# Optimization experiments

Measured on AMD Instinct MI355X. Metric: run time of the kernel, lower is better.

The kernel has to match this reference:

```python
import jax, jax.numpy as jnp
import numpy as np


def soft_thresholding(x, a):
    # sh(x, a) = max(0, |x| - a) * sign(x) == relu(x - a) - relu(-x - a)
    return jax.nn.relu(x - a) - jax.nn.relu(-x - a)


def setup_inputs() -> dict:
    key = jax.random.key(0)
    kA, kb = jax.random.split(key)
    bs, m, n = 32, 256, 512
    A = jax.random.normal(kA, (bs, m, n), dtype=jnp.float32)
    b = jax.random.normal(kb, (bs, m), dtype=jnp.float32)
    return {"A": A, "b": b, "bs": bs, "iters": 1000}


def reference(A, b, bs, iters, alpha=0.02, beta=0.02):
    # A: (bs, m, n), b: (bs, m). PDHG iteration:
    #   x = sh(x - alpha * A^T u, alpha)
    m, n = A.shape[1], A.shape[2]
    x0 = jnp.zeros((bs, n), dtype=jnp.float32)
    u0 = jnp.zeros((bs, m), dtype=jnp.float32)

    def step(carry, _):
        x, u = carry
        x_new = soft_thresholding(x - alpha * jnp.einsum('bmn,bm->bn', A, u), alpha)
        u_new = u + beta * (jnp.einsum('bmn,bn->bm', A, 2.0 * x_new - x) - b)
        return (x_new, u_new), None

    (x, u), _ = jax.lax.scan(step, (x0, u0), None, length=iters)
    return x
```

## Files before the change

### kernel.cpp

```cpp
#include <hip/hip_runtime.h>

#define BS    32
#define MDIM  256
#define NDIM  512
#define ITERS 1000
#define WPB   4
#define RPW   128
#define BLK   512
#define ALPHA 0.02f
#define BETA  0.02f

#define ATS        516
#define ATILE_FL   (32 * ATS)
#define WBUF_OFF   ATILE_FL
#define WBLK       20
#define P_OFF      (WBUF_OFF + 32 * WBLK)
#define C_OFF      (P_OFF + RPW * 32)
#define BT_OFF     (C_OFF + RPW)
#define SMEM_FL    (BT_OFF + 32)

#define SLAB_FL   (2 * BS * NDIM)

__device__ __forceinline__ unsigned ld_coh_u32(const void* p) {
  return __hip_atomic_load(reinterpret_cast<const unsigned*>(p),
                           __ATOMIC_RELAXED, __HIP_MEMORY_SCOPE_AGENT);
}
__device__ __forceinline__ void st_coh_u32(void* p, unsigned v) {
  __hip_atomic_store(reinterpret_cast<unsigned*>(p), v,
                     __ATOMIC_RELAXED, __HIP_MEMORY_SCOPE_AGENT);
}
__device__ __forceinline__ unsigned tagf(float v, unsigned tag) {
  return (__float_as_uint(v) & ~0xFFu) | tag;
}

__global__ __launch_bounds__(BLK, 1) void pdhg_kernel(
    const float* __restrict__ A, const float* __restrict__ Bvec,
    float* __restrict__ out, float* __restrict__ slab)
{
  __shared__ float smem[SMEM_FL];
  const int tid   = threadIdx.x;
  const int bid   = blockIdx.x;
  const int batch = bid & (BS - 1);
  const int slice = bid >> 5;
  const int i0    = slice * RPW;

  const int tj = tid & 31;
  const int ti = tid >> 5;

  float acc[8][16];
#pragma unroll
  for (int r = 0; r < 8; ++r)
#pragma unroll
    for (int s = 0; s < 16; ++s) acc[r][s] = 0.f;
  float cacc[8];
#pragma unroll
  for (int r = 0; r < 8; ++r) cacc[r] = 0.f;

  const float* Ag = A + (size_t)batch * MDIM * NDIM;

  for (int mt = 0; mt < MDIM / 32; ++mt) {
#pragma unroll 4
    for (int q = 0; q < 8; ++q) {
      int f  = q * 512 + tid;
      int mm = f >> 7;
      int j  = (f & 127) << 2;
      float4 v = *reinterpret_cast<const float4*>(
          Ag + (size_t)(mt * 32 + mm) * NDIM + j);
      *reinterpret_cast<float4*>(
          &smem[(j >> 4) * ATS + mm * 16 + (j & 15)]) = v;
    }
    if (tid < 32) smem[BT_OFF + tid] = Bvec[batch * MDIM + mt * 32 + tid];
    __syncthreads();

    const int ibase = ((i0 + 8 * ti) >> 4) * ATS + ((8 * ti) & 15);
    const int jbase = tj * ATS;
    for (int mm = 0; mm < 32; ++mm) {
      float4 a0 = *reinterpret_cast<const float4*>(&smem[ibase + mm * 16]);
      float4 a1 = *reinterpret_cast<const float4*>(&smem[ibase + mm * 16 + 4]);
      float ai[8] = {a0.x, a0.y, a0.z, a0.w, a1.x, a1.y, a1.z, a1.w};
      float aj[16];
#pragma unroll
      for (int kk = 0; kk < 4; ++kk) {
        float4 v = *reinterpret_cast<const float4*>(
            &smem[jbase + mm * 16 + 4 * kk]);
        aj[4*kk] = v.x; aj[4*kk+1] = v.y; aj[4*kk+2] = v.z; aj[4*kk+3] = v.w;
      }
#pragma unroll
      for (int r = 0; r < 8; ++r)
#pragma unroll
        for (int s = 0; s < 16; ++s) acc[r][s] = fmaf(ai[r], aj[s], acc[r][s]);
      if (tj == 0) {
        float bv = smem[BT_OFF + mm];
#pragma unroll
        for (int r = 0; r < 8; ++r) cacc[r] = fmaf(ai[r], bv, cacc[r]);
      }
    }
    __syncthreads();
  }
  if (tj == 0) {
#pragma unroll
    for (int r = 0; r < 8; ++r) smem[C_OFF + ti * 8 + r] = cacc[r];
  }
  __syncthreads();

  const bool owner   = (tid & 3) == 0;
  const int  i_own   = tid >> 2;
  const float c_reg  = smem[C_OFF + i_own];
  float x = 0.f, t = 0.f;

  float* myslot = slab + batch * NDIM + i0 + i_own;
  const float* myrd = slab + batch * NDIM + tid;

  for (int k = 0; k < ITERS; ++k) {
    float xn = 0.f;
    if (owner) {
      float y = x - ALPHA * t;
      xn = fmaxf(y - ALPHA, 0.f) - fmaxf(-y - ALPHA, 0.f);
    }
    if (k == ITERS - 1) { x = xn; break; }

    const int par = (k & 1) * BS * NDIM;
    const unsigned tag = (unsigned)(k + 1) & 0xFFu;
    if (owner) {
      float wv = 2.f * xn - x;
      x = xn;
      st_coh_u32(myslot + par, tagf(wv, tag));
    }

    unsigned qq;
    do {
      qq = ld_coh_u32(myrd + par);
    } while ((qq ^ tag) & 0xFFu);

    smem[WBUF_OFF + (tid >> 4) * WBLK + (tid & 15)] = __uint_as_float(qq);
    __syncthreads();

    float wv[16];
    {
      const float* wb = &smem[WBUF_OFF + tj * WBLK];
#pragma unroll
      for (int kk = 0; kk < 4; ++kk) {
        float4 v = *reinterpret_cast<const float4*>(wb + 4 * kk);
        wv[4*kk] = v.x; wv[4*kk+1] = v.y; wv[4*kk+2] = v.z; wv[4*kk+3] = v.w;
      }
    }
#pragma unroll
    for (int r = 0; r < 8; ++r) {
      float p = 0.f;
#pragma unroll
      for (int s = 0; s < 16; ++s) p = fmaf(acc[r][s], wv[s], p);
      smem[P_OFF + (ti * 8 + r) * 32 + tj] = p;
    }
    __syncthreads();

    {
      int ired = tid >> 2, prt = tid & 3;
      const float* pp = &smem[P_OFF + ired * 32 + prt * 8];
      float4 pa = *reinterpret_cast<const float4*>(pp);
      float4 pb = *reinterpret_cast<const float4*>(pp + 4);
      float s8 = (pa.x + pa.y) + (pa.z + pa.w) +
                 (pb.x + pb.y) + (pb.z + pb.w);
      s8 += __shfl_xor(s8, 1);
      s8 += __shfl_xor(s8, 2);
      if (owner) t += BETA * (s8 - c_reg);
    }
  }

  if (owner) out[(size_t)batch * NDIM + i0 + i_own] = x;
}

extern "C" void kernel_launch(void* const* d_in, const int* in_sizes, int n_in,
                              void* d_out, int out_size, void* d_ws, size_t ws_size,
                              hipStream_t stream) {
  const float* A = (const float*)d_in[0];
  const float* b = (const float*)d_in[1];
  float* out  = (float*)d_out;
  float* slab = (float*)d_ws;

  hipMemsetAsync(d_ws, 0, SLAB_FL * sizeof(float), stream);

  void* args[] = {(void*)&A, (void*)&b, (void*)&out, (void*)&slab};
  hipLaunchCooperativeKernel((const void*)pdhg_kernel, dim3(BS * WPB), dim3(BLK),
                             args, 0, stream);
}
```

Baseline: 1.553 ms.

## Replace shared-memory partial-sum reduction with butterfly shuffles and double-buffer w

```diff
diff --git a/kernel.cpp b/kernel.cpp
--- a/kernel.cpp
+++ b/kernel.cpp
@@ -10,16 +10,15 @@
 #define ALPHA 0.02f
 #define BETA  0.02f
 
-#define ATS        516
-#define ATILE_FL   (32 * ATS)
-#define WBUF_OFF   ATILE_FL
-#define WBLK       20
-#define P_OFF      (WBUF_OFF + 32 * WBLK)
-#define C_OFF      (P_OFF + RPW * 32)
-#define BT_OFF     (C_OFF + RPW)
-#define SMEM_FL    (BT_OFF + 32)
-
-#define SLAB_FL   (2 * BS * NDIM)
+#define ATS      516
+#define ATILE_FL (32 * ATS)
+#define WBUF_OFF ATILE_FL
+#define WBLK     20
+#define C_OFF    (WBUF_OFF + 2 * 32 * WBLK)
+#define BT_OFF   (C_OFF + RPW)
+#define SMEM_FL  (BT_OFF + 32)
+
+#define SLAB_FL  (2 * BS * NDIM)
 
 __device__ __forceinline__ unsigned ld_coh_u32(const void* p) {
   return __hip_atomic_load(reinterpret_cast<const unsigned*>(p),
@@ -44,8 +43,9 @@
   const int slice = bid >> 5;
   const int i0    = slice * RPW;
 
-  const int tj = tid & 31;
-  const int ti = tid >> 5;
+  const int tj   = tid & 31;
+  const int ti   = tid >> 5;
+  const int lane = tid & 63;
 
   float acc[8][16];
 #pragma unroll
@@ -103,12 +103,14 @@
   }
   __syncthreads();
 
-  const bool owner   = (tid & 3) == 0;
-  const int  i_own   = tid >> 2;
-  const float c_reg  = smem[C_OFF + i_own];
+  const int  r_of  = ((lane >> 4) & 1) * 4 + ((lane >> 3) & 1) * 2 +
+                     ((lane >> 2) & 1);
+  const int  i_loc = ti * 8 + r_of;
+  const bool owner = (lane & 3) == 0;
+  const float c_reg = smem[C_OFF + i_loc];
   float x = 0.f, t = 0.f;
 
-  float* myslot = slab + batch * NDIM + i0 + i_own;
+  float* myslot = slab + batch * NDIM + i0 + i_loc;
   const float* myrd = slab + batch * NDIM + tid;
 
   for (int k = 0; k < ITERS; ++k) {
@@ -122,9 +124,9 @@
     const int par = (k & 1) * BS * NDIM;
     const unsigned tag = (unsigned)(k + 1) & 0xFFu;
     if (owner) {
-      float wv = 2.f * xn - x;
+      float wv_pub = 2.f * xn - x;
       x = xn;
-      st_coh_u32(myslot + par, tagf(wv, tag));
+      st_coh_u32(myslot + par, tagf(wv_pub, tag));
     }
 
     unsigned qq;
@@ -132,41 +134,56 @@
       qq = ld_coh_u32(myrd + par);
     } while ((qq ^ tag) & 0xFFu);
 
-    smem[WBUF_OFF + (tid >> 4) * WBLK + (tid & 15)] = __uint_as_float(qq);
+    float* wst = &smem[WBUF_OFF + (k & 1) * (32 * WBLK)];
+    wst[(tid >> 4) * WBLK + (tid & 15)] = __uint_as_float(qq);
     __syncthreads();
 
     float wv[16];
     {
-      const float* wb = &smem[WBUF_OFF + tj * WBLK];
+      const float* wb = &wst[tj * WBLK];
 #pragma unroll
       for (int kk = 0; kk < 4; ++kk) {
         float4 v = *reinterpret_cast<const float4*>(wb + 4 * kk);
         wv[4*kk] = v.x; wv[4*kk+1] = v.y; wv[4*kk+2] = v.z; wv[4*kk+3] = v.w;
       }
     }
+    float p[8];
 #pragma unroll
     for (int r = 0; r < 8; ++r) {
-      float p = 0.f;
-#pragma unroll
-      for (int s = 0; s < 16; ++s) p = fmaf(acc[r][s], wv[s], p);
-      smem[P_OFF + (ti * 8 + r) * 32 + tj] = p;
-    }
-    __syncthreads();
-
+      float pv = 0.f;
+#pragma unroll
+      for (int s = 0; s < 16; ++s) pv = fmaf(acc[r][s], wv[s], pv);
+      p[r] = pv;
+    }
+
+    const bool b4 = (lane & 16), b3 = (lane & 8), b2 = (lane & 4);
+    float n[4];
+#pragma unroll
+    for (int q = 0; q < 4; ++q) {
+      float s_ = b4 ? p[q] : p[q + 4];
+      float rv = __shfl_xor(s_, 16);
+      n[q] = (b4 ? p[q + 4] : p[q]) + rv;
+    }
+    float m2[2];
+#pragma unroll
+    for (int q = 0; q < 2; ++q) {
+      float s_ = b3 ? n[q] : n[q + 2];
+      float rv = __shfl_xor(s_, 8);
+      m2[q] = (b3 ? n[q + 2] : n[q]) + rv;
+    }
+    float v1;
     {
-      int ired = tid >> 2, prt = tid & 3;
-      const float* pp = &smem[P_OFF + ired * 32 + prt * 8];
-      float4 pa = *reinterpret_cast<const float4*>(pp);
-      float4 pb = *reinterpret_cast<const float4*>(pp + 4);
-      float s8 = (pa.x + pa.y) + (pa.z + pa.w) +
-                 (pb.x + pb.y) + (pb.z + pb.w);
-      s8 += __shfl_xor(s8, 1);
-      s8 += __shfl_xor(s8, 2);
-      if (owner) t += BETA * (s8 - c_reg);
-    }
+      float s_ = b2 ? m2[0] : m2[1];
+      float rv = __shfl_xor(s_, 4);
+      v1 = (b2 ? m2[1] : m2[0]) + rv;
+    }
+    v1 += __shfl_xor(v1, 2);
+    v1 += __shfl_xor(v1, 1);
+
+    if (owner) t += BETA * (v1 - c_reg);
   }
 
-  if (owner) out[(size_t)batch * NDIM + i0 + i_own] = x;
+  if (owner) out[(size_t)batch * NDIM + i0 + i_loc] = x;
 }
 
 extern "C" void kernel_launch(void* const* d_in, const int* in_sizes, int n_in,
```

Result: no change. 1.556 ms (+0.2%).
